# Kernel optimization log

Hardware: AMD Instinct MI355X
Metric: run time of the kernel (lower is better)

## Reference

```python
import jax, jax.numpy as jnp
import numpy as np

DN = ('NCDHW', 'OIDHW', 'NCDHW')

def conv3d(x, w, stride, padding):
    return jax.lax.conv_general_dilated(x, w, window_strides=stride, padding=padding, dimension_numbers=DN)

def swish(v):
    return v * jax.nn.sigmoid(v)

def setup_inputs() -> dict:
    key = jax.random.key(0)
    ks = jax.random.split(key, 16)
    B, Cin, Cout, E, D, H, W = 4, 64, 128, 256, 8, 128, 128
    r = lambda k, shp, s=0.05: jax.random.normal(k, shp, dtype=jnp.float32) * s
    return {
        'x': jax.random.normal(ks[0], (B, Cin, D, H, W), dtype=jnp.float32),
        'embed': jax.random.normal(ks[1], (B, E), dtype=jnp.float32),
        'context': jax.random.normal(ks[2], (B, E), dtype=jnp.float32),
        'w20': r(ks[3], (Cout, Cin, 3, 3, 3)),
        'b20': r(ks[4], (Cout,)),
        'w21': r(ks[5], (Cout, Cout, 3, 3, 3)),
        'd1_w': r(ks[6], (E, Cin)),
        'd1_b': r(ks[7], (Cin,)),
        'd2_w': r(ks[8], (E, Cout)),
        'd2_b': r(ks[9], (Cout,)),
        'res_w': r(ks[10], (Cout, Cin, 1, 1, 1)),
        'res_b': r(ks[11], (Cout,)),
        'down_w': r(ks[12], (Cout, Cout, 3, 3, 3)),
        'down_b': r(ks[13], (Cout,)),
    }

def reference(x, embed, context, w20, b20, w21, d1_w, d1_b, d2_w, d2_b, res_w, res_b, down_w, down_b):
    # --- ResBlockModulateBEST ---
    s1 = embed @ d1_w + d1_b                       # (B, Cin) time-embedding shift
    h = swish(x + s1[:, :, None, None, None])
    # dropout is identity in eval/reference mode
    h = conv3d(h, w20, (1, 1, 1), [(1, 1), (1, 1), (1, 1)]) + b20[None, :, None, None, None]
    h = swish(h)
    # modulated_conv3d: s scales the IN-channel axis of w21 per sample; since conv is
    # linear in its input channels this equals conv3d(h * s, w21) — same math, no
    # per-sample grouped conv needed.
    s2 = context @ d2_w + d2_b                     # (B, Cout == Cin of conv21)
    h = conv3d(h * s2[:, :, None, None, None], w21, (1, 1, 1), [(1, 1), (1, 1), (1, 1)])
    res = conv3d(x, res_w, (1, 1, 1), [(0, 0), (0, 0), (0, 0)]) + res_b[None, :, None, None, None]
    h = h + res
    # --- down path ---
    h = swish(h)
    out = conv3d(h, down_w, (1, 2, 2), [(1, 1), (0, 0), (0, 0)]) + down_b[None, :, None, None, None]
    return out  # (B, Cout, D, (H-3)//2+1, (W-3)//2+1) = (4,128,8,63,63)
```

## Files before the change

kernel.cpp:

```cpp
#include <hip/hip_runtime.h>
#include <cstdint>
#include <cstddef>

typedef __attribute__((ext_vector_type(8))) short bf16x8;
typedef __attribute__((ext_vector_type(4))) short bf16x4v;
typedef __attribute__((ext_vector_type(4))) float f32x4;

__device__ inline short f2bf(float f) {
  union { float f; unsigned u; } c; c.f = f;
  unsigned u = c.u;
  unsigned r = (u + 0x7fffu + ((u >> 16) & 1u)) >> 16;
  return (short)r;
}
__device__ inline float swish_f(float v) { return v / (1.f + __expf(-v)); }

__device__ inline void gld_lds16(const void* g, void* l) {
  __builtin_amdgcn_global_load_lds((const __attribute__((address_space(1))) void*)g,
                                   (__attribute__((address_space(3))) void*)l, 16, 0, 0);
}

#define ACQ(VM) do {                                                     \
    asm volatile("s_waitcnt vmcnt(" VM ")" ::: "memory");                \
    __builtin_amdgcn_s_barrier();                                        \
    asm volatile("" ::: "memory");                                       \
  } while (0)
#define REL() do {                                                       \
    asm volatile("" ::: "memory");                                       \
    __builtin_amdgcn_s_barrier();                                        \
  } while (0)

__global__ __launch_bounds__(256) void scales_kernel(
    const float* __restrict__ embed, const float* __restrict__ context,
    const float* __restrict__ d1w, const float* __restrict__ d1b,
    const float* __restrict__ d2w, const float* __restrict__ d2b,
    float* __restrict__ s1, float* __restrict__ s2) {
  int tid = blockIdx.x * 256 + threadIdx.x;
  if (tid < 256) {
    int b = tid >> 6, c = tid & 63;
    float acc = d1b[c];
    for (int e = 0; e < 256; ++e) acc += embed[b * 256 + e] * d1w[e * 64 + c];
    s1[tid] = acc;
  } else if (tid < 768) {
    int o = tid - 256;
    int b = o >> 7, c = o & 127;
    float acc = d2b[c];
    for (int e = 0; e < 256; ++e) acc += context[b * 256 + e] * d2w[e * 128 + c];
    s2[o] = acc;
  }
}

__global__ __launch_bounds__(256) void prep_w_kernel(
    const float* __restrict__ w20, const float* __restrict__ w21,
    const float* __restrict__ wdn, const float* __restrict__ rsw,
    short* __restrict__ wt20, short* __restrict__ wt21,
    short* __restrict__ wtdn, short* __restrict__ rw) {
  for (int o = blockIdx.x * 256 + threadIdx.x; o < 1114112; o += gridDim.x * 256) {
    if (o < 221184) {
      int t = o >> 13, rem = o & 8191, co = rem >> 6, ci = rem & 63;
      wt20[o] = f2bf(w20[(co * 64 + ci) * 27 + t]);
    } else if (o < 663552) {
      int p = o - 221184;
      int t = p >> 14, rem = p & 16383, co = rem >> 7, ci = rem & 127;
      wt21[p] = f2bf(w21[(co * 128 + ci) * 27 + t]);
    } else if (o < 1105920) {
      int p = o - 663552;
      int t = p >> 14, rem = p & 16383, co = rem >> 7, ci = rem & 127;
      wtdn[p] = f2bf(wdn[(co * 128 + ci) * 27 + t]);
    } else {
      int p = o - 1105920;
      rw[p] = f2bf(rsw[p]);
    }
  }
}

__global__ __launch_bounds__(256) void prep_h1_kernel(
    const float* __restrict__ xin, const float* __restrict__ s1,
    short* __restrict__ h1) {
  __shared__ __align__(16) short sm[128 * 72];
  const int tid = threadIdx.x;
  const int gid = blockIdx.x;
  const int y = gid & 127, z = (gid >> 7) & 7, b = gid >> 10;
  const float* xbase = xin + (size_t)b * 8388608 + (size_t)z * 16384 + (size_t)y * 128;
#pragma unroll
  for (int i = 0; i < 8; ++i) {
    int e = i * 256 + tid;
    int ci = e >> 5, x4 = e & 31;
    float4 v = *(const float4*)(xbase + (size_t)ci * 131072 + x4 * 4);
    float s = s1[b * 64 + ci];
    sm[(x4 * 4 + 0) * 72 + ci] = f2bf(swish_f(v.x + s));
    sm[(x4 * 4 + 1) * 72 + ci] = f2bf(swish_f(v.y + s));
    sm[(x4 * 4 + 2) * 72 + ci] = f2bf(swish_f(v.z + s));
    sm[(x4 * 4 + 3) * 72 + ci] = f2bf(swish_f(v.w + s));
  }
  __syncthreads();
  short* orow = h1 + (size_t)gid * 8192;
#pragma unroll
  for (int i = 0; i < 4; ++i) {
    int e = i * 256 + tid;
    int xx = e >> 3, c8 = e & 7;
    *(bf16x8*)(orow + e * 8) = *(const bf16x8*)(&sm[xx * 72 + c8 * 8]);
  }
}

__global__ __launch_bounds__(256, 3) void conv20_kernel(
    const short* __restrict__ h1, const short* __restrict__ wt,
    const float* __restrict__ b20, const float* __restrict__ s2,
    short* __restrict__ h2) {
  __shared__ __align__(16) short sm[24704];
  const int tid = threadIdx.x;
  const int bi = blockIdx.x;
  const int xcd = bi & 7, slot = bi >> 3;
  const int yo = slot & 15, z = (slot >> 4) & 7, b = slot >> 7;
  const int y = xcd * 16 + yo;
  const int gid = b * 1024 + z * 128 + y;
  const int lane = tid & 63, wave = tid >> 6;
  const int wm = wave >> 1, wn = wave & 1;
  const int q = lane >> 4, n0 = lane & 15;
  const bf16x8 zz = {0, 0, 0, 0, 0, 0, 0, 0};
  short* inbuf = sm;
  f32x4 acc[4][4];
#pragma unroll
  for (int i = 0; i < 4; ++i)
#pragma unroll
    for (int j = 0; j < 4; ++j) acc[i][j] = (f32x4){0.f, 0.f, 0.f, 0.f};

  auto wstage = [&](int s) {
    const short* src = wt + (s << 13);
    short* dst = sm + 8320 + ((s & 1) << 13);
    int r = lane >> 3, ss = lane & 7;
#pragma unroll
    for (int i = 0; i < 4; ++i) {
      int c = wave * 4 + i;
      gld_lds16(src + ((c * 8 + r) << 6) + ((ss ^ r) << 3), dst + (c << 9));
    }
  };
  auto instage = [&](int it) {
    int kz = it / 3, ky = it - kz * 3;
    int zi = z + kz - 1, yi = y + ky - 1;
    if (zi >= 0 && zi < 8 && yi >= 0 && yi < 128) {
      const short* row = h1 + ((size_t)(b * 1024 + zi * 128 + yi) << 13);
#pragma unroll
      for (int i = 0; i < 4; ++i) {
        int x0 = 1 + 8 * (wave * 4 + i);
        int x = x0 + (lane >> 3);
        int c8 = (lane & 7) ^ (x & 7);
        gld_lds16(row + ((x - 1) << 6) + (c8 << 3), inbuf + (x0 << 6));
      }
    } else {
#pragma unroll
      for (int i = 0; i < 4; ++i)
        *(bf16x8*)(&inbuf[64 + (i * 256 + tid) * 8]) = zz;
      asm volatile("s_waitcnt lgkmcnt(0)" ::: "memory");
    }
  };

  if (tid < 16) {
    int hf = tid >> 3, u = tid & 7;
    *(bf16x8*)(&inbuf[(hf ? 129 : 0) * 64 + u * 8]) = zz;
  }
  wstage(0);
  instage(0);
  __syncthreads();

  for (int s = 0; s < 27; ++s) {
    const int it3 = s / 3, kx = s - it3 * 3;
    if (s < 26) wstage(s + 1);
    if (s < 26) ACQ("4"); else ACQ("0");
    const short* w = sm + 8320 + ((s & 1) << 13);
    bf16x8 af[2][4], bb[2][4];
#pragma unroll
    for (int ch = 0; ch < 2; ++ch) {
#pragma unroll
      for (int i = 0; i < 4; ++i)
        af[ch][i] = *(const bf16x8*)(&w[(wm * 64 + i * 16 + n0) * 64 + (((ch * 4 + q) ^ (n0 & 7)) << 3)]);
#pragma unroll
      for (int j = 0; j < 4; ++j) {
        int xx = wn * 64 + j * 16 + n0 + kx;
        bb[ch][j] = *(const bf16x8*)(&inbuf[xx * 64 + (((ch * 4 + q) ^ (xx & 7)) << 3)]);
      }
    }
    __builtin_amdgcn_s_setprio(1);
#pragma unroll
    for (int ch = 0; ch < 2; ++ch)
#pragma unroll
      for (int i = 0; i < 4; ++i)
#pragma unroll
        for (int j = 0; j < 4; ++j)
          acc[i][j] = __builtin_amdgcn_mfma_f32_16x16x32_bf16(af[ch][i], bb[ch][j], acc[i][j], 0, 0, 0);
    __builtin_amdgcn_s_setprio(0);
    REL();
    if (kx == 2 && it3 < 8) instage(it3 + 1);
  }
#pragma unroll
  for (int i = 0; i < 4; ++i) {
    const int mb = wm * 64 + i * 16 + q * 4;
    const float4 bias = *(const float4*)(b20 + mb);
    const float4 sc = *(const float4*)(s2 + b * 128 + mb);
#pragma unroll
    for (int j = 0; j < 4; ++j) {
      const int n = wn * 64 + j * 16 + n0;
      bf16x4v pk;
      pk.x = f2bf(swish_f(acc[i][j][0] + bias.x) * sc.x);
      pk.y = f2bf(swish_f(acc[i][j][1] + bias.y) * sc.y);
      pk.z = f2bf(swish_f(acc[i][j][2] + bias.z) * sc.z);
      pk.w = f2bf(swish_f(acc[i][j][3] + bias.w) * sc.w);
      *(bf16x4v*)(&sm[n * 136 + mb]) = pk;
    }
  }
  __syncthreads();
  short* orow = h2 + (size_t)gid * 16384;
#pragma unroll
  for (int i = 0; i < 8; ++i) {
    int e = i * 256 + tid;
    int xx = e >> 4, c8 = e & 15;
    *(bf16x8*)(orow + e * 8) = *(const bf16x8*)(&sm[xx * 136 + c8 * 8]);
  }
}

__global__ __launch_bounds__(256, 2) void conv21_kernel(
    const short* __restrict__ h2, const short* __restrict__ wt,
    const float* __restrict__ xin, const short* __restrict__ rw,
    const float* __restrict__ res_b, short* __restrict__ h3) {
  __shared__ __align__(16) short sm[33024];
  const int tid = threadIdx.x;
  const int bi = blockIdx.x;
  const int xcd = bi & 7, slot = bi >> 3;
  const int yo = slot & 15, z = (slot >> 4) & 7, b = slot >> 7;
  const int y = xcd * 16 + yo;
  const int gid = b * 1024 + z * 128 + y;
  const int lane = tid & 63, wave = tid >> 6;
  const int wm = wave >> 1, wn = wave & 1;
  const int q = lane >> 4, n0 = lane & 15;
  const bf16x8 zz = {0, 0, 0, 0, 0, 0, 0, 0};
  short* inbuf = sm;
  f32x4 acc[4][4];
#pragma unroll
  for (int i = 0; i < 4; ++i)
#pragma unroll
    for (int j = 0; j < 4; ++j) acc[i][j] = (f32x4){0.f, 0.f, 0.f, 0.f};

  auto wstage = [&](int s) {
    int it6 = s / 6, sub = s - it6 * 6, kx = sub >> 1, ch2 = sub & 1;
    const short* src = wt + (((it6 * 3 + kx) << 14) + (ch2 << 6));
    short* dst = sm + 16640 + ((s & 1) << 13);
    int r = lane >> 3, ss = lane & 7;
#pragma unroll
    for (int i = 0; i < 4; ++i) {
      int c = wave * 4 + i;
      gld_lds16(src + ((c * 8 + r) << 7) + ((ss ^ r) << 3), dst + (c << 9));
    }
  };
  auto instage = [&](int it) {
    int kz = it / 3, ky = it - kz * 3;
    int zi = z + kz - 1, yi = y + ky - 1;
    if (zi >= 0 && zi < 8 && yi >= 0 && yi < 128) {
      const short* row = h2 + ((size_t)(b * 1024 + zi * 128 + yi) << 14);
#pragma unroll
      for (int i = 0; i < 8; ++i) {
        int x0 = 1 + 4 * (wave * 8 + i);
        int x = x0 + (lane >> 4);
        int c8 = (lane & 15) ^ (x & 15);
        gld_lds16(row + ((x - 1) << 7) + (c8 << 3), inbuf + (x0 << 7));
      }
    } else {
#pragma unroll
      for (int i = 0; i < 8; ++i)
        *(bf16x8*)(&inbuf[128 + (i * 256 + tid) * 8]) = zz;
      asm volatile("s_waitcnt lgkmcnt(0)" ::: "memory");
    }
  };

  if (tid < 32) {
    int hf = tid >> 4, u = tid & 15;
    *(bf16x8*)(&inbuf[(hf ? 129 : 0) * 128 + u * 8]) = zz;
  }
  wstage(0);
  instage(0);
  __syncthreads();

  float4 xv[8];
  for (int s = 0; s < 54; ++s) {
    const int it6 = s / 6, sub = s - it6 * 6, kx = sub >> 1, ch2 = sub & 1;
    if (s < 53) wstage(s + 1);
    if (s == 52)      ACQ("12");
    else if (s == 53) ACQ("0");
    else              ACQ("4");
    if (s == 51) {
      const float* xb = xin + (size_t)b * 8388608 + (size_t)z * 16384 + (size_t)y * 128;
#pragma unroll
      for (int i = 0; i < 8; ++i) {
        int e = i * 256 + tid;
        int ci = e >> 5, x4 = e & 31;
        xv[i] = *(const float4*)(xb + (size_t)ci * 131072 + x4 * 4);
      }
    }
    const short* w = sm + 16640 + ((s & 1) << 13);
    bf16x8 af[2][4], bb[2][4];
#pragma unroll
    for (int chL = 0; chL < 2; ++chL) {
      const int ch = ch2 * 2 + chL;
#pragma unroll
      for (int i = 0; i < 4; ++i)
        af[chL][i] = *(const bf16x8*)(&w[(wm * 64 + i * 16 + n0) * 64 + (((chL * 4 + q) ^ (n0 & 7)) << 3)]);
#pragma unroll
      for (int j = 0; j < 4; ++j) {
        int xx = wn * 64 + j * 16 + n0 + kx;
        bb[chL][j] = *(const bf16x8*)(&inbuf[(xx << 7) + (((ch * 4 + q) ^ (xx & 15)) << 3)]);
      }
    }
    __builtin_amdgcn_s_setprio(1);
#pragma unroll
    for (int chL = 0; chL < 2; ++chL)
#pragma unroll
      for (int i = 0; i < 4; ++i)
#pragma unroll
        for (int j = 0; j < 4; ++j)
          acc[i][j] = __builtin_amdgcn_mfma_f32_16x16x32_bf16(af[chL][i], bb[chL][j], acc[i][j], 0, 0, 0);
    __builtin_amdgcn_s_setprio(0);
    REL();
    if (sub == 5 && it6 < 8) instage(it6 + 1);
  }
  short* rbuf = sm + 16640;
  {
#pragma unroll
    for (int i = 0; i < 8; ++i) {
      int e = i * 256 + tid;
      int ci = e >> 5, x4 = e & 31;
      int u0 = ci >> 3, cl = ci & 7;
#pragma unroll
      for (int k = 0; k < 4; ++k) {
        int xx = x4 * 4 + k;
        float fv = (k == 0) ? xv[i].x : (k == 1) ? xv[i].y : (k == 2) ? xv[i].z : xv[i].w;
        rbuf[xx * 64 + ((u0 ^ (xx & 7) ^ ((xx >> 3) & 7)) << 3) + cl] = f2bf(fv);
      }
    }
  }
  __syncthreads();
#pragma unroll
  for (int ch = 0; ch < 2; ++ch) {
    bf16x8 af[4], bb[4];
#pragma unroll
    for (int i = 0; i < 4; ++i)
      af[i] = *(const bf16x8*)(rw + (wm * 64 + i * 16 + n0) * 64 + ch * 32 + q * 8);
#pragma unroll
    for (int j = 0; j < 4; ++j) {
      int xx = wn * 64 + j * 16 + n0;
      bb[j] = *(const bf16x8*)(&rbuf[xx * 64 + (((ch * 4 + q) ^ (xx & 7) ^ ((xx >> 3) & 7)) << 3)]);
    }
#pragma unroll
    for (int i = 0; i < 4; ++i)
#pragma unroll
      for (int j = 0; j < 4; ++j)
        acc[i][j] = __builtin_amdgcn_mfma_f32_16x16x32_bf16(af[i], bb[j], acc[i][j], 0, 0, 0);
  }
  __syncthreads();
#pragma unroll
  for (int i = 0; i < 4; ++i) {
    const int mb = wm * 64 + i * 16 + q * 4;
    const float4 bias = *(const float4*)(res_b + mb);
#pragma unroll
    for (int j = 0; j < 4; ++j) {
      const int n = wn * 64 + j * 16 + n0;
      bf16x4v pk;
      pk.x = f2bf(swish_f(acc[i][j][0] + bias.x));
      pk.y = f2bf(swish_f(acc[i][j][1] + bias.y));
      pk.z = f2bf(swish_f(acc[i][j][2] + bias.z));
      pk.w = f2bf(swish_f(acc[i][j][3] + bias.w));
      *(bf16x4v*)(&sm[n * 136 + mb]) = pk;
    }
  }
  __syncthreads();
  short* orow = h3 + (size_t)gid * 16384;
#pragma unroll
  for (int i = 0; i < 8; ++i) {
    int e = i * 256 + tid;
    int xx = e >> 4, c8 = e & 15;
    *(bf16x8*)(orow + e * 8) = *(const bf16x8*)(&sm[xx * 136 + c8 * 8]);
  }
}

__global__ __launch_bounds__(256, 2) void down_kernel(
    const short* __restrict__ h3, const short* __restrict__ wt,
    const float* __restrict__ dnb, float* __restrict__ out) {
  __shared__ __align__(16) short sm[33024];
  const int tid = threadIdx.x;
  const int bi = blockIdx.x;
  const int o = (bi & 7) * 252 + (bi >> 3);
  const int yo = o % 63;
  const int zb = o / 63;
  const int z = zb & 7, b = zb >> 3;
  const int lane = tid & 63, wave = tid >> 6;
  const int wm = wave >> 1, wn = wave & 1;
  const int q = lane >> 4, n0 = lane & 15;
  const bf16x8 zz = {0, 0, 0, 0, 0, 0, 0, 0};
  short* inbuf = sm;
  f32x4 acc[4][2];
#pragma unroll
  for (int i = 0; i < 4; ++i)
#pragma unroll
    for (int j = 0; j < 2; ++j) acc[i][j] = (f32x4){0.f, 0.f, 0.f, 0.f};

  auto wstage = [&](int s) {
    int it6 = s / 6, sub = s - it6 * 6, kx = sub >> 1, ch2 = sub & 1;
    const short* src = wt + (((it6 * 3 + kx) << 14) + (ch2 << 6));
    short* dst = sm + 16640 + ((s & 1) << 13);
    int r = lane >> 3, ss = lane & 7;
#pragma unroll
    for (int i = 0; i < 4; ++i) {
      int c = wave * 4 + i;
      gld_lds16(src + ((c * 8 + r) << 7) + ((ss ^ r) << 3), dst + (c << 9));
    }
  };
  auto instage = [&](int it) {
    int kz = it / 3, ky = it - kz * 3;
    int zi = z + kz - 1;
    int yi = 2 * yo + ky;
    if (zi >= 0 && zi < 8) {
      const short* row = h3 + ((size_t)(b * 1024 + zi * 128 + yi) << 14);
#pragma unroll
      for (int i = 0; i < 8; ++i) {
        int x0 = 4 * (wave * 8 + i);
        int x = x0 + (lane >> 4);
        int c8 = (lane & 15) ^ (x & 15);
        gld_lds16(row + (x << 7) + (c8 << 3), inbuf + (x0 << 7));
      }
    } else {
#pragma unroll
      for (int i = 0; i < 8; ++i)
        *(bf16x8*)(&inbuf[(i * 256 + tid) * 8]) = zz;
      asm volatile("s_waitcnt lgkmcnt(0)" ::: "memory");
    }
  };

  if (tid < 32) {
    int hf = tid >> 4, u = tid & 15;
    *(bf16x8*)(&inbuf[(128 + hf) * 128 + u * 8]) = zz;
  }
  wstage(0);
  instage(0);
  __syncthreads();

  for (int s = 0; s < 54; ++s) {
    const int it6 = s / 6, sub = s - it6 * 6, kx = sub >> 1, ch2 = sub & 1;
    if (s < 53) wstage(s + 1);
    if (s < 53) ACQ("4"); else ACQ("0");
    const short* w = sm + 16640 + ((s & 1) << 13);
    bf16x8 af[2][4], bb[2][2];
#pragma unroll
    for (int chL = 0; chL < 2; ++chL) {
      const int ch = ch2 * 2 + chL;
#pragma unroll
      for (int i = 0; i < 4; ++i)
        af[chL][i] = *(const bf16x8*)(&w[(wm * 64 + i * 16 + n0) * 64 + (((chL * 4 + q) ^ (n0 & 7)) << 3)]);
#pragma unroll
      for (int j = 0; j < 2; ++j) {
        int xp = 2 * (wn * 32 + j * 16 + n0) + kx;
        bb[chL][j] = *(const bf16x8*)(&inbuf[(xp << 7) + (((ch * 4 + q) ^ (xp & 15)) << 3)]);
      }
    }
    __builtin_amdgcn_s_setprio(1);
#pragma unroll
    for (int chL = 0; chL < 2; ++chL)
#pragma unroll
      for (int i = 0; i < 4; ++i)
#pragma unroll
        for (int j = 0; j < 2; ++j)
          acc[i][j] = __builtin_amdgcn_mfma_f32_16x16x32_bf16(af[chL][i], bb[chL][j], acc[i][j], 0, 0, 0);
    __builtin_amdgcn_s_setprio(0);
    REL();
    if (sub == 5 && it6 < 8) instage(it6 + 1);
  }
  float* fsm = (float*)sm;
#pragma unroll
  for (int i = 0; i < 4; ++i) {
    const int mb = wm * 64 + i * 16 + q * 4;
    const float4 bias = *(const float4*)(dnb + mb);
#pragma unroll
    for (int j = 0; j < 2; ++j) {
      const int n = wn * 32 + j * 16 + n0;
      f32x4 v;
      v[0] = acc[i][j][0] + bias.x;
      v[1] = acc[i][j][1] + bias.y;
      v[2] = acc[i][j][2] + bias.z;
      v[3] = acc[i][j][3] + bias.w;
      *(f32x4*)(&fsm[n * 132 + mb]) = v;
    }
  }
  __syncthreads();
#pragma unroll
  for (int it = 0; it < 32; ++it) {
    int idx = it * 256 + tid;
    int co = idx >> 6, xl = idx & 63;
    if (xl < 63)
      out[((size_t)(b * 128 + co) * 8 + z) * 3969 + yo * 63 + xl] = fsm[xl * 132 + co];
  }
}

extern "C" void kernel_launch(void* const* d_in, const int* in_sizes, int n_in,
                              void* d_out, int out_size, void* d_ws, size_t ws_size,
                              hipStream_t stream) {
  const float* x       = (const float*)d_in[0];
  const float* embed   = (const float*)d_in[1];
  const float* context = (const float*)d_in[2];
  const float* w20     = (const float*)d_in[3];
  const float* b20     = (const float*)d_in[4];
  const float* w21     = (const float*)d_in[5];
  const float* d1w     = (const float*)d_in[6];
  const float* d1b     = (const float*)d_in[7];
  const float* d2w     = (const float*)d_in[8];
  const float* d2b     = (const float*)d_in[9];
  const float* resw    = (const float*)d_in[10];
  const float* resb    = (const float*)d_in[11];
  const float* dnw     = (const float*)d_in[12];
  const float* dnb     = (const float*)d_in[13];
  float* out = (float*)d_out;
  char* ws = (char*)d_ws;
  float* s1   = (float*)(ws + 0);
  float* s2   = (float*)(ws + 1024);
  short* wt20 = (short*)(ws + 4096);
  short* wt21 = (short*)(ws + 446464);
  short* wtdn = (short*)(ws + 1331200);
  short* rw   = (short*)(ws + 2215936);
  short* h1   = (short*)(ws + 2232320);
  short* h2   = (short*)(ws + 69341184);
  short* h3   = (short*)(ws + 203558912);

  scales_kernel<<<3, 256, 0, stream>>>(embed, context, d1w, d1b, d2w, d2b, s1, s2);
  prep_w_kernel<<<1088, 256, 0, stream>>>(w20, w21, dnw, resw, wt20, wt21, wtdn, rw);
  prep_h1_kernel<<<4096, 256, 0, stream>>>(x, s1, h1);
  conv20_kernel<<<4096, 256, 0, stream>>>(h1, wt20, b20, s2, h2);
  conv21_kernel<<<4096, 256, 0, stream>>>(h2, wt21, x, rw, resb, h3);
  down_kernel<<<2016, 256, 0, stream>>>(h3, wtdn, dnb, out);
}
```

Baseline: 1.008 ms.

## Prefetch next-step B fragments into double-buffered registers across conv main loops

Restructures the three convolution main loops so the B-operand (input tile) LDS reads for the next K-step are issued one step ahead into alternating register sets (bbA/bbB). The loops are grouped by each staged input row and end with explicit epilogue steps. The goal is to overlap LDS fragment latency with MFMA work instead of reading and consuming fragments in the same step. It also changes the fp32 output staging stride from 132 to 133 to reduce LDS bank conflicts. The cost is higher register pressure, and 16-byte vector stores at an odd stride may become unaligned.

```diff
diff --git a/kernel.cpp b/kernel.cpp
--- a/kernel.cpp
+++ b/kernel.cpp
@@ -153,6 +153,34 @@
       asm volatile("s_waitcnt lgkmcnt(0)" ::: "memory");
     }
   };
+  auto rd_af = [&](int par, bf16x8 (&af)[2][4]) {
+    const short* w = sm + 8320 + (par << 13);
+#pragma unroll
+    for (int ch = 0; ch < 2; ++ch)
+#pragma unroll
+      for (int i = 0; i < 4; ++i)
+        af[ch][i] = *(const bf16x8*)(&w[(wm * 64 + i * 16 + n0) * 64 + (((ch * 4 + q) ^ (n0 & 7)) << 3)]);
+  };
+  auto rd_bb = [&](int kx, bf16x8 (&bb)[2][4]) {
+#pragma unroll
+    for (int ch = 0; ch < 2; ++ch)
+#pragma unroll
+      for (int j = 0; j < 4; ++j) {
+        int xx = wn * 64 + j * 16 + n0 + kx;
+        bb[ch][j] = *(const bf16x8*)(&inbuf[xx * 64 + (((ch * 4 + q) ^ (xx & 7)) << 3)]);
+      }
+  };
+  auto domfma = [&](bf16x8 (&af)[2][4], bf16x8 (&bb)[2][4]) {
+    __builtin_amdgcn_s_setprio(1);
+#pragma unroll
+    for (int ch = 0; ch < 2; ++ch)
+#pragma unroll
+      for (int i = 0; i < 4; ++i)
+#pragma unroll
+        for (int j = 0; j < 4; ++j)
+          acc[i][j] = __builtin_amdgcn_mfma_f32_16x16x32_bf16(af[ch][i], bb[ch][j], acc[i][j], 0, 0, 0);
+    __builtin_amdgcn_s_setprio(0);
+  };
 
   if (tid < 16) {
     int hf = tid >> 3, u = tid & 7;
@@ -162,34 +190,31 @@
   instage(0);
   __syncthreads();
 
-  for (int s = 0; s < 27; ++s) {
-    const int it3 = s / 3, kx = s - it3 * 3;
-    if (s < 26) wstage(s + 1);
-    if (s < 26) ACQ("4"); else ACQ("0");
-    const short* w = sm + 8320 + ((s & 1) << 13);
-    bf16x8 af[2][4], bb[2][4];
-#pragma unroll
-    for (int ch = 0; ch < 2; ++ch) {
-#pragma unroll
-      for (int i = 0; i < 4; ++i)
-        af[ch][i] = *(const bf16x8*)(&w[(wm * 64 + i * 16 + n0) * 64 + (((ch * 4 + q) ^ (n0 & 7)) << 3)]);
-#pragma unroll
-      for (int j = 0; j < 4; ++j) {
-        int xx = wn * 64 + j * 16 + n0 + kx;
-        bb[ch][j] = *(const bf16x8*)(&inbuf[xx * 64 + (((ch * 4 + q) ^ (xx & 7)) << 3)]);
-      }
-    }
-    __builtin_amdgcn_s_setprio(1);
-#pragma unroll
-    for (int ch = 0; ch < 2; ++ch)
-#pragma unroll
-      for (int i = 0; i < 4; ++i)
-#pragma unroll
-        for (int j = 0; j < 4; ++j)
-          acc[i][j] = __builtin_amdgcn_mfma_f32_16x16x32_bf16(af[ch][i], bb[ch][j], acc[i][j], 0, 0, 0);
-    __builtin_amdgcn_s_setprio(0);
-    REL();
-    if (kx == 2 && it3 < 8) instage(it3 + 1);
+  bf16x8 af[2][4], bbA[2][4], bbB[2][4];
+  for (int g = 0; g < 8; ++g) {
+#pragma unroll
+    for (int u = 0; u < 3; ++u) {
+      const int s = g * 3 + u;
+      wstage(s + 1);
+      ACQ("4");
+      rd_af(s & 1, af);
+      if (u == 0) rd_bb(0, bbA);
+      if (u == 0) rd_bb(1, bbB);
+      if (u == 1) rd_bb(2, bbA);
+      domfma(af, (u & 1) ? bbB : bbA);
+      REL();
+      if (u == 2) instage(g + 1);
+    }
+  }
+  {
+    wstage(25); ACQ("4"); rd_af(0, af);
+    rd_bb(0, bbA); rd_bb(1, bbB);
+    domfma(af, bbA); REL();
+    wstage(26); ACQ("4"); rd_af(1, af);
+    rd_bb(2, bbA);
+    domfma(af, bbB); REL();
+    ACQ("0"); rd_af(0, af);
+    domfma(af, bbA); REL();
   }
 #pragma unroll
   for (int i = 0; i < 4; ++i) {
@@ -269,6 +294,36 @@
       asm volatile("s_waitcnt lgkmcnt(0)" ::: "memory");
     }
   };
+  auto rd_af = [&](int par, bf16x8 (&af)[2][4]) {
+    const short* w = sm + 16640 + (par << 13);
+#pragma unroll
+    for (int chL = 0; chL < 2; ++chL)
+#pragma unroll
+      for (int i = 0; i < 4; ++i)
+        af[chL][i] = *(const bf16x8*)(&w[(wm * 64 + i * 16 + n0) * 64 + (((chL * 4 + q) ^ (n0 & 7)) << 3)]);
+  };
+  auto rd_bb = [&](int kx, int ch2, bf16x8 (&bb)[2][4]) {
+#pragma unroll
+    for (int chL = 0; chL < 2; ++chL) {
+      const int ch = ch2 * 2 + chL;
+#pragma unroll
+      for (int j = 0; j < 4; ++j) {
+        int xx = wn * 64 + j * 16 + n0 + kx;
+        bb[chL][j] = *(const bf16x8*)(&inbuf[(xx << 7) + (((ch * 4 + q) ^ (xx & 15)) << 3)]);
+      }
+    }
+  };
+  auto domfma = [&](bf16x8 (&af)[2][4], bf16x8 (&bb)[2][4]) {
+    __builtin_amdgcn_s_setprio(1);
+#pragma unroll
+    for (int chL = 0; chL < 2; ++chL)
+#pragma unroll
+      for (int i = 0; i < 4; ++i)
+#pragma unroll
+        for (int j = 0; j < 4; ++j)
+          acc[i][j] = __builtin_amdgcn_mfma_f32_16x16x32_bf16(af[chL][i], bb[chL][j], acc[i][j], 0, 0, 0);
+    __builtin_amdgcn_s_setprio(0);
+  };
 
   if (tid < 32) {
     int hf = tid >> 4, u = tid & 15;
@@ -278,14 +333,34 @@
   instage(0);
   __syncthreads();
 
+  bf16x8 af[2][4], bbA[2][4], bbB[2][4];
   float4 xv[8];
-  for (int s = 0; s < 54; ++s) {
-    const int it6 = s / 6, sub = s - it6 * 6, kx = sub >> 1, ch2 = sub & 1;
-    if (s < 53) wstage(s + 1);
-    if (s == 52)      ACQ("12");
-    else if (s == 53) ACQ("0");
-    else              ACQ("4");
-    if (s == 51) {
+  for (int g = 0; g < 8; ++g) {
+#pragma unroll
+    for (int u = 0; u < 6; ++u) {
+      const int s = g * 6 + u;
+      wstage(s + 1);
+      ACQ("4");
+      rd_af(u & 1, af);
+      if (u == 0) rd_bb(0, 0, bbA);
+      if (u < 5) rd_bb((u + 1) >> 1, (u + 1) & 1, (u & 1) ? bbA : bbB);
+      domfma(af, (u & 1) ? bbB : bbA);
+      REL();
+      if (u == 5) instage(g + 1);
+    }
+  }
+  {
+    wstage(49); ACQ("4"); rd_af(0, af);
+    rd_bb(0, 0, bbA); rd_bb(0, 1, bbB);
+    domfma(af, bbA); REL();
+    wstage(50); ACQ("4"); rd_af(1, af);
+    rd_bb(1, 0, bbA);
+    domfma(af, bbB); REL();
+    wstage(51); ACQ("4"); rd_af(0, af);
+    rd_bb(1, 1, bbB);
+    domfma(af, bbA); REL();
+    wstage(52); ACQ("4");
+    {
       const float* xb = xin + (size_t)b * 8388608 + (size_t)z * 16384 + (size_t)y * 128;
 #pragma unroll
       for (int i = 0; i < 8; ++i) {
@@ -294,31 +369,16 @@
         xv[i] = *(const float4*)(xb + (size_t)ci * 131072 + x4 * 4);
       }
     }
-    const short* w = sm + 16640 + ((s & 1) << 13);
-    bf16x8 af[2][4], bb[2][4];
-#pragma unroll
-    for (int chL = 0; chL < 2; ++chL) {
-      const int ch = ch2 * 2 + chL;
-#pragma unroll
-      for (int i = 0; i < 4; ++i)
-        af[chL][i] = *(const bf16x8*)(&w[(wm * 64 + i * 16 + n0) * 64 + (((chL * 4 + q) ^ (n0 & 7)) << 3)]);
-#pragma unroll
-      for (int j = 0; j < 4; ++j) {
-        int xx = wn * 64 + j * 16 + n0 + kx;
-        bb[chL][j] = *(const bf16x8*)(&inbuf[(xx << 7) + (((ch * 4 + q) ^ (xx & 15)) << 3)]);
-      }
-    }
-    __builtin_amdgcn_s_setprio(1);
-#pragma unroll
-    for (int chL = 0; chL < 2; ++chL)
-#pragma unroll
-      for (int i = 0; i < 4; ++i)
-#pragma unroll
-        for (int j = 0; j < 4; ++j)
-          acc[i][j] = __builtin_amdgcn_mfma_f32_16x16x32_bf16(af[chL][i], bb[chL][j], acc[i][j], 0, 0, 0);
-    __builtin_amdgcn_s_setprio(0);
-    REL();
-    if (sub == 5 && it6 < 8) instage(it6 + 1);
+    rd_af(1, af);
+    rd_bb(2, 0, bbA);
+    domfma(af, bbB); REL();
+    wstage(53); ACQ("12");
+    rd_af(0, af);
+    rd_bb(2, 1, bbB);
+    domfma(af, bbA); REL();
+    ACQ("0");
+    rd_af(1, af);
+    domfma(af, bbB); REL();
   }
   short* rbuf = sm + 16640;
   {
@@ -338,20 +398,20 @@
   __syncthreads();
 #pragma unroll
   for (int ch = 0; ch < 2; ++ch) {
-    bf16x8 af[4], bb[4];
+    bf16x8 raf[4], rbb[4];
 #pragma unroll
     for (int i = 0; i < 4; ++i)
-      af[i] = *(const bf16x8*)(rw + (wm * 64 + i * 16 + n0) * 64 + ch * 32 + q * 8);
+      raf[i] = *(const bf16x8*)(rw + (wm * 64 + i * 16 + n0) * 64 + ch * 32 + q * 8);
 #pragma unroll
     for (int j = 0; j < 4; ++j) {
       int xx = wn * 64 + j * 16 + n0;
-      bb[j] = *(const bf16x8*)(&rbuf[xx * 64 + (((ch * 4 + q) ^ (xx & 7) ^ ((xx >> 3) & 7)) << 3)]);
+      rbb[j] = *(const bf16x8*)(&rbuf[xx * 64 + (((ch * 4 + q) ^ (xx & 7) ^ ((xx >> 3) & 7)) << 3)]);
     }
 #pragma unroll
     for (int i = 0; i < 4; ++i)
 #pragma unroll
       for (int j = 0; j < 4; ++j)
-        acc[i][j] = __builtin_amdgcn_mfma_f32_16x16x32_bf16(af[i], bb[j], acc[i][j], 0, 0, 0);
+        acc[i][j] = __builtin_amdgcn_mfma_f32_16x16x32_bf16(raf[i], rbb[j], acc[i][j], 0, 0, 0);
   }
   __syncthreads();
 #pragma unroll
@@ -431,6 +491,36 @@
       asm volatile("s_waitcnt lgkmcnt(0)" ::: "memory");
     }
   };
+  auto rd_af = [&](int par, bf16x8 (&af)[2][4]) {
+    const short* w = sm + 16640 + (par << 13);
+#pragma unroll
+    for (int chL = 0; chL < 2; ++chL)
+#pragma unroll
+      for (int i = 0; i < 4; ++i)
+        af[chL][i] = *(const bf16x8*)(&w[(wm * 64 + i * 16 + n0) * 64 + (((chL * 4 + q) ^ (n0 & 7)) << 3)]);
+  };
+  auto rd_bb = [&](int kx, int ch2, bf16x8 (&bb)[2][2]) {
+#pragma unroll
+    for (int chL = 0; chL < 2; ++chL) {
+      const int ch = ch2 * 2 + chL;
+#pragma unroll
+      for (int j = 0; j < 2; ++j) {
+        int xp = 2 * (wn * 32 + j * 16 + n0) + kx;
+        bb[chL][j] = *(const bf16x8*)(&inbuf[(xp << 7) + (((ch * 4 + q) ^ (xp & 15)) << 3)]);
+      }
+    }
+  };
+  auto domfma = [&](bf16x8 (&af)[2][4], bf16x8 (&bb)[2][2]) {
+    __builtin_amdgcn_s_setprio(1);
+#pragma unroll
+    for (int chL = 0; chL < 2; ++chL)
+#pragma unroll
+      for (int i = 0; i < 4; ++i)
+#pragma unroll
+        for (int j = 0; j < 2; ++j)
+          acc[i][j] = __builtin_amdgcn_mfma_f32_16x16x32_bf16(af[chL][i], bb[chL][j], acc[i][j], 0, 0, 0);
+    __builtin_amdgcn_s_setprio(0);
+  };
 
   if (tid < 32) {
     int hf = tid >> 4, u = tid & 15;
@@ -440,35 +530,39 @@
   instage(0);
   __syncthreads();
 
-  for (int s = 0; s < 54; ++s) {
-    const int it6 = s / 6, sub = s - it6 * 6, kx = sub >> 1, ch2 = sub & 1;
-    if (s < 53) wstage(s + 1);
-    if (s < 53) ACQ("4"); else ACQ("0");
-    const short* w = sm + 16640 + ((s & 1) << 13);
-    bf16x8 af[2][4], bb[2][2];
-#pragma unroll
-    for (int chL = 0; chL < 2; ++chL) {
-      const int ch = ch2 * 2 + chL;
-#pragma unroll
-      for (int i = 0; i < 4; ++i)
-        af[chL][i] = *(const bf16x8*)(&w[(wm * 64 + i * 16 + n0) * 64 + (((chL * 4 + q) ^ (n0 & 7)) << 3)]);
-#pragma unroll
-      for (int j = 0; j < 2; ++j) {
-        int xp = 2 * (wn * 32 + j * 16 + n0) + kx;
-        bb[chL][j] = *(const bf16x8*)(&inbuf[(xp << 7) + (((ch * 4 + q) ^ (xp & 15)) << 3)]);
-      }
-    }
-    __builtin_amdgcn_s_setprio(1);
-#pragma unroll
-    for (int chL = 0; chL < 2; ++chL)
-#pragma unroll
-      for (int i = 0; i < 4; ++i)
-#pragma unroll
-        for (int j = 0; j < 2; ++j)
-          acc[i][j] = __builtin_amdgcn_mfma_f32_16x16x32_bf16(af[chL][i], bb[chL][j], acc[i][j], 0, 0, 0);
-    __builtin_amdgcn_s_setprio(0);
-    REL();
-    if (sub == 5 && it6 < 8) instage(it6 + 1);
+  bf16x8 af[2][4], bbA[2][2], bbB[2][2];
+  for (int g = 0; g < 8; ++g) {
+#pragma unroll
+    for (int u = 0; u < 6; ++u) {
+      const int s = g * 6 + u;
+      wstage(s + 1);
+      ACQ("4");
+      rd_af(u & 1, af);
+      if (u == 0) rd_bb(0, 0, bbA);
+      if (u < 5) rd_bb((u + 1) >> 1, (u + 1) & 1, (u & 1) ? bbA : bbB);
+      domfma(af, (u & 1) ? bbB : bbA);
+      REL();
+      if (u == 5) instage(g + 1);
+    }
+  }
+  {
+    wstage(49); ACQ("4"); rd_af(0, af);
+    rd_bb(0, 0, bbA); rd_bb(0, 1, bbB);
+    domfma(af, bbA); REL();
+    wstage(50); ACQ("4"); rd_af(1, af);
+    rd_bb(1, 0, bbA);
+    domfma(af, bbB); REL();
+    wstage(51); ACQ("4"); rd_af(0, af);
+    rd_bb(1, 1, bbB);
+    domfma(af, bbA); REL();
+    wstage(52); ACQ("4"); rd_af(1, af);
+    rd_bb(2, 0, bbA);
+    domfma(af, bbB); REL();
+    wstage(53); ACQ("4"); rd_af(0, af);
+    rd_bb(2, 1, bbB);
+    domfma(af, bbA); REL();
+    ACQ("0"); rd_af(1, af);
+    domfma(af, bbB); REL();
   }
   float* fsm = (float*)sm;
 #pragma unroll
@@ -483,7 +577,7 @@
       v[1] = acc[i][j][1] + bias.y;
       v[2] = acc[i][j][2] + bias.z;
       v[3] = acc[i][j][3] + bias.w;
-      *(f32x4*)(&fsm[n * 132 + mb]) = v;
+      *(f32x4*)(&fsm[n * 133 + mb]) = v;
     }
   }
   __syncthreads();
@@ -492,7 +586,7 @@
     int idx = it * 256 + tid;
     int co = idx >> 6, xl = idx & 63;
     if (xl < 63)
-      out[((size_t)(b * 128 + co) * 8 + z) * 3969 + yo * 63 + xl] = fsm[xl * 132 + co];
+      out[((size_t)(b * 128 + co) * 8 + z) * 3969 + yo * 63 + xl] = fsm[xl * 133 + co];
   }
 }
 
```

New measurement: 1.402 ms. +39.1%, slower.
